# Performance work log

Measured on AMD Instinct MI355X. Metric: run time of the kernel, lower is better.

## Reference

```python
import jax, jax.numpy as jnp
import numpy as np
from jax import lax


def _conv(x, w, b, pad, dil):
    # standard NCHW conv, OIHW weights
    y = lax.conv_general_dilated(x, w, (1, 1), [(pad, pad), (pad, pad)],
                                 rhs_dilation=(dil, dil),
                                 dimension_numbers=('NCHW', 'OIHW', 'NCHW'))
    return y + b[None, :, None, None]


def _bilinear(img, py, px):
    # img: [B,C,H,W]; py,px: [B,KK,H,W] float sample positions.
    # Zero-padding bilinear sampling (torchvision deform_conv semantics):
    # each of the 4 corners contributes 0 if it lies outside the image.
    B, C, H, W = img.shape
    y0 = jnp.floor(py)
    x0 = jnp.floor(px)
    wy1 = py - y0
    wx1 = px - x0
    imgf = img.reshape(B, C, H * W)

    def corner(yi, xi, wgt):
        valid = (yi >= 0) & (yi <= H - 1) & (xi >= 0) & (xi <= W - 1)
        yc = jnp.clip(yi, 0, H - 1).astype(jnp.int32)
        xc = jnp.clip(xi, 0, W - 1).astype(jnp.int32)
        idx = yc * W + xc  # [B,KK,H,W]
        g = jax.vmap(lambda im, ix: jnp.take(im, ix.reshape(-1), axis=1))(imgf, idx)
        g = g.reshape(B, C, *yi.shape[1:])  # [B,C,KK,H,W]
        return g * (wgt * valid.astype(img.dtype))[:, None]

    return (corner(y0, x0, (1 - wy1) * (1 - wx1))
            + corner(y0, x0 + 1, (1 - wy1) * wx1)
            + corner(y0 + 1, x0, wy1 * (1 - wx1))
            + corner(y0 + 1, x0 + 1, wy1 * wx1))


def _deform_dw(x, off_w, off_b, dw_w, K, pad, dil):
    # offset-predicted deformable depthwise conv (groups == channels)
    B, C, H, W = x.shape
    off = _conv(x, off_w, off_b, pad, dil).reshape(B, K * K, 2, H, W)
    dy, dx = off[:, :, 0], off[:, :, 1]  # torchvision order: (dy, dx) per tap
    ky, kx = jnp.meshgrid(jnp.arange(K), jnp.arange(K), indexing='ij')
    by = (ky.reshape(-1) * dil - pad).astype(x.dtype)  # [KK]
    bx = (kx.reshape(-1) * dil - pad).astype(x.dtype)
    py = jnp.arange(H, dtype=x.dtype)[None, None, :, None] + by[None, :, None, None] + dy
    px = jnp.arange(W, dtype=x.dtype)[None, None, None, :] + bx[None, :, None, None] + dx
    s = _bilinear(x, py, px)  # [B,C,KK,H,W]
    return jnp.einsum('bckhw,ck->bchw', s, dw_w.reshape(C, K * K))


def setup_inputs() -> dict:
    key = jax.random.key(0)
    ks = jax.random.split(key, 9)
    B, C, H, W = 4, 64, 56, 56
    f = lambda k, shape, s: jax.random.normal(k, shape, jnp.float32) * s
    return dict(
        x=f(ks[0], (B, C, H, W), 1.0),
        off_w1=f(ks[1], (2 * 5 * 5, C, 5, 5), 0.01), off_b1=f(ks[2], (2 * 5 * 5,), 0.01),
        dw_w1=f(ks[3], (C, 1, 5, 5), 0.1),
        off_w2=f(ks[4], (2 * 7 * 7, C, 7, 7), 0.01), off_b2=f(ks[5], (2 * 7 * 7,), 0.01),
        dw_w2=f(ks[6], (C, 1, 7, 7), 0.1),
        pw_w=f(ks[7], (C, C, 1, 1), 0.05), pw_b=f(ks[8], (C,), 0.05),
    )


def reference(x, off_w1, off_b1, dw_w1, off_w2, off_b2, dw_w2, pw_w, pw_b):
    attn = _deform_dw(x, off_w1, off_b1, dw_w1, 5, 2, 1)       # 5x5 deformable dw
    attn = _deform_dw(attn, off_w2, off_b2, dw_w2, 7, 9, 3)    # 7x7 dil-3 deformable dw
    attn = _conv(attn, pw_w, pw_b, 0, 1)                       # 1x1 pointwise
    return x * attn                                            # gated multiply
```

## Files before the change

### kernel.cpp

```cpp
#include <hip/hip_runtime.h>

#define BB 4
#define CC 64
#define HH 56
#define WW 56
#define HW (HH*WW)

typedef unsigned short u16;
typedef unsigned int u32;
typedef __attribute__((ext_vector_type(8))) short bf16x8;
typedef __attribute__((ext_vector_type(4))) float f32x4;

__device__ __forceinline__ u16 f2bf(float f) {
    union { float f; unsigned u; } c; c.f = f;
    unsigned u = c.u;
    u = (u + 0x7FFFu + ((u >> 16) & 1u)) >> 16;
    return (u16)u;
}
__device__ __forceinline__ float bf2f(u16 v) {
    union { unsigned u; float f; } c; c.u = ((unsigned)v) << 16;
    return c.f;
}
__device__ __forceinline__ float lo_f(u32 u) {
    union { unsigned u; float f; } c; c.u = u << 16; return c.f;
}
__device__ __forceinline__ float hi_f(u32 u) {
    union { unsigned u; float f; } c; c.u = u & 0xffff0000u; return c.f;
}

#define R1 102400
#define R2 401408
#define R3 4096
#define R4 1600
#define R5 3136
#define TGRID (BB*(HW/64))
#define PREPN (R1+R2+R3+R4+R5)
__global__ __launch_bounds__(256)
void prep_tr_kernel(const float* __restrict__ x,
                    const float* __restrict__ ow1, const float* __restrict__ ow2,
                    const float* __restrict__ pw,  const float* __restrict__ dw1,
                    const float* __restrict__ dw2,
                    u16* __restrict__ xT,
                    u16* __restrict__ w2t1, u16* __restrict__ w2t2,
                    u16* __restrict__ pwT, float* __restrict__ dwT1,
                    float* __restrict__ dwT2) {
    __shared__ u16 tile[64][72];
    const int t = threadIdx.x;
    if (blockIdx.x < TGRID) {
        const int blk = blockIdx.x;
        const int b   = blk / (HW/64);
        const int p0  = (blk % (HW/64))*64;
        const int px  = t & 63, icq = t >> 6;
        const float* ip = x + ((size_t)b*CC + icq*16)*HW + p0 + px;
        #pragma unroll
        for (int i = 0; i < 16; ++i)
            tile[px][icq*16 + i] = f2bf(ip[(size_t)i*HW]);
        __syncthreads();
        const int px2 = t >> 2, g = t & 3;
        u16* op = xT + ((size_t)b*HW + p0 + px2)*64 + g*16;
        const uint4* s = (const uint4*)&tile[px2][g*16];
        ((uint4*)op)[0] = s[0];
        ((uint4*)op)[1] = s[1];
        return;
    }
    const int i = (blockIdx.x - TGRID)*256 + t;
    if (i < R1) {
        const int ic = i & 63, n = (i >> 6) & 63, tap = i >> 12;
        w2t1[i] = f2bf((n < 50) ? ow1[((size_t)n*64 + ic)*25 + tap] : 0.f);
    } else if (i < R1+R2) {
        const int j = i - R1;
        const int ic = j & 63, n = (j >> 6) & 127, tap = j >> 13;
        w2t2[j] = f2bf((n < 98) ? ow2[((size_t)n*64 + ic)*49 + tap] : 0.f);
    } else if (i < R1+R2+R3) {
        const int j = i - (R1+R2);
        pwT[j] = f2bf(pw[j]);
    } else if (i < R1+R2+R3+R4) {
        const int j = i - (R1+R2+R3);
        const int c = j & 63, k = j >> 6;
        dwT1[j] = dw1[c*25 + k];
    } else if (i < R1+R2+R3+R4+R5) {
        const int j = i - (R1+R2+R3+R4);
        const int c = j & 63, k = j >> 6;
        dwT2[j] = dw2[c*49 + k];
    }
}

__device__ __forceinline__ uint4 selz(bool v, uint4 a) {
    const uint4 z = make_uint4(0,0,0,0);
    return v ? a : z;
}

template<int K, int DIL, int PAD, int COUT, int NP, int NPAD, int NTW>
__global__ __launch_bounds__(256, 4)
void conv_mfma_lds_kernel(const u16* __restrict__ xT, const u16* __restrict__ w2t,
                          const float* __restrict__ bias, float* __restrict__ out) {
    constexpr int KK = K*K;
    constexpr int BROWS = 16*NTW;
    __shared__ u16 Ab[2][64*64];
    __shared__ u16 Bb[2][BROWS*64];

    const int nm   = HW/64;
    const int b    = blockIdx.x / nm;
    const int p0   = (blockIdx.x % nm)*64;
    const int nt0  = blockIdx.y;
    const int t    = threadIdx.x;
    const int wave = t >> 6;
    const int lane = t & 63;

    const int spx = t >> 3;
    const int sc  = t & 7;
    const int pA  = p0 + spx;
    const int pB  = p0 + spx + 32;
    const int pyA = pA / WW, pxA = pA % WW;
    const int pyB = pB / WW, pxB = pB % WW;
    const u16* xb = xT + (size_t)b*HW*64;
    const int sslotA = ((sc + spx) & 7)*8;
    const int bn  = t >> 3;
    const int bslot = ((sc + bn) & 7)*8;
    const u16* wbase = w2t + (size_t)nt0*BROWS*64;

    const int r = lane & 15, quad = lane >> 4;
    const int mloc = wave*16 + r;
    const int arow = mloc*64;
    const int a0s = ((quad     + mloc) & 7)*8;
    const int a1s = ((quad + 4 + mloc) & 7)*8;
    const int b0s = ((quad     + r) & 7)*8;
    const int b1s = ((quad + 4 + r) & 7)*8;

    f32x4 acc[NTW];
    #pragma unroll
    for (int h = 0; h < NTW; ++h) acc[h] = (f32x4){0.f,0.f,0.f,0.f};
    const uint4 z4 = make_uint4(0,0,0,0);

    auto LD = [&](int tap, uint4& a0, uint4& a1, bool& va, bool& vb, uint4& bb) {
        const int dyy = (tap/K)*DIL - PAD;
        const int dxx = (tap%K)*DIL - PAD;
        const int off = dyy*WW + dxx;
        {
            const int yy = pyA + dyy, xx = pxA + dxx;
            va = ((unsigned)yy < (unsigned)HH) && ((unsigned)xx < (unsigned)WW);
            a0 = *(const uint4*)(xb + (size_t)(va ? (pA + off) : 0)*64 + sc*8);
        }
        {
            const int yy = pyB + dyy, xx = pxB + dxx;
            vb = ((unsigned)yy < (unsigned)HH) && ((unsigned)xx < (unsigned)WW);
            a1 = *(const uint4*)(xb + (size_t)(vb ? (pB + off) : 0)*64 + sc*8);
        }
        if (BROWS == 32 || bn < BROWS)
            bb = *(const uint4*)(wbase + ((size_t)tap*NP + bn)*64 + sc*8);
    };

    uint4 rA0 = z4, rA1 = z4, rB = z4;
    bool v0 = false, v1 = false;
    LD(0, rA0, rA1, v0, v1, rB);

    #pragma unroll
    for (int tap = 0; tap < KK; ++tap) {
        uint4 nA0 = z4, nA1 = z4, nB = z4;
        bool nv0 = false, nv1 = false;
        if (tap + 1 < KK) LD(tap + 1, nA0, nA1, nv0, nv1, nB);

        u16* A  = &Ab[tap & 1][0];
        u16* Bq = &Bb[tap & 1][0];
        *(uint4*)(A + spx*64      + sslotA) = selz(v0, rA0);
        *(uint4*)(A + (spx+32)*64 + sslotA) = selz(v1, rA1);
        if (BROWS == 32 || bn < BROWS) *(uint4*)(Bq + bn*64 + bslot) = rB;
        __syncthreads();

        const bf16x8 av0 = *(const bf16x8*)(A + arow + a0s);
        const bf16x8 av1 = *(const bf16x8*)(A + arow + a1s);
        #pragma unroll
        for (int h = 0; h < NTW; ++h) {
            const int brow = (h*16 + r)*64;
            const bf16x8 bv0 = *(const bf16x8*)(Bq + brow + b0s);
            const bf16x8 bv1 = *(const bf16x8*)(Bq + brow + b1s);
            acc[h] = __builtin_amdgcn_mfma_f32_16x16x32_bf16(av0, bv0, acc[h], 0, 0, 0);
            acc[h] = __builtin_amdgcn_mfma_f32_16x16x32_bf16(av1, bv1, acc[h], 0, 0, 0);
        }

        rA0 = nA0; rA1 = nA1; rB = nB; v0 = nv0; v1 = nv1;
    }

    #pragma unroll
    for (int h = 0; h < NTW; ++h) {
        const int n = nt0*BROWS + h*16 + r;
        if (n < COUT) {
            const float bv = bias[n];
            float* op = out + ((size_t)b*HW + p0 + wave*16 + quad*4)*NPAD + n;
            #pragma unroll
            for (int r2 = 0; r2 < 4; ++r2) op[(size_t)r2*NPAD] = acc[h][r2] + bv;
        }
    }
}

template<int K, int DIL, int PAD, int NPAD>
__global__ __launch_bounds__(256)
void deform_cl_kernel(const u16* __restrict__ inT, const float* __restrict__ offT,
                      const float* __restrict__ dwT, u16* __restrict__ outT) {
    constexpr int KK = K*K;
    __shared__ float4 swt[8][KK];
    __shared__ int4   sat[8][KK];
    __shared__ float  sdw[KK*64];

    const int t = threadIdx.x;
    const int nb8 = (BB*HW/8) >> 3;
    const int blk0 = blockIdx.x;
    const int blk = (blk0 & 7)*nb8 + (blk0 >> 3);
    const int p0 = blk*8;
    const int b  = p0 / HW;
    const int pl0 = p0 - b*HW;

    for (int i = t; i < KK*64; i += 256) sdw[i] = dwT[i];

    for (int i = t; i < 8*KK; i += 256) {
        const int pix = i / KK, k = i - pix*KK;
        const int pl  = pl0 + pix;
        const int h = pl / WW, w = pl % WW;
        const float* orow = offT + ((size_t)b*HW + pl)*NPAD;
        const float dy = orow[2*k];
        const float dx = orow[2*k+1];
        const float py = (float)(h + (k/K)*DIL - PAD) + dy;
        const float px = (float)(w + (k%K)*DIL - PAD) + dx;
        const float y0f = floorf(py), x0f = floorf(px);
        const float wy1 = py - y0f,  wx1 = px - x0f;
        const float wy0 = 1.f - wy1, wx0 = 1.f - wx1;
        const int y0 = (int)y0f, x0 = (int)x0f;

        const int y0c = min(max(y0,   0), HH-1);
        const int y1c = min(max(y0+1, 0), HH-1);
        const int x0c = min(max(x0,   0), WW-1);
        const int x1c = min(max(x0+1, 0), WW-1);
        const float gy0 = wy0 * ((y0   >= 0 && y0   < HH) ? 1.f : 0.f);
        const float gy1 = wy1 * ((y0+1 >= 0 && y0+1 < HH) ? 1.f : 0.f);
        const float gx0 = wx0 * ((x0   >= 0 && x0   < WW) ? 1.f : 0.f);
        const float gx1 = wx1 * ((x0+1 >= 0 && x0+1 < WW) ? 1.f : 0.f);

        swt[pix][k] = make_float4(gy0*gx0, gy0*gx1, gy1*gx0, gy1*gx1);
        const int r0 = y0c*WW, r1 = y1c*WW;
        sat[pix][k] = make_int4((r0 + x0c) << 7, (r0 + x1c) << 7,
                                (r1 + x0c) << 7, (r1 + x1c) << 7);
    }
    __syncthreads();

    const int wave = t >> 6, lane = t & 63;
    const int pixl = 2*wave + (lane >> 5);
    const int chp  = lane & 31;
    const char* ib = (const char*)(inT + (size_t)b*HW*64) + chp*4;

    float accx = 0.f, accy = 0.f;

    int4   av[3];
    float4 wv[2];
    float2 dv[2];
    u32 c00[2], c01[2], c10[2], c11[2];

    av[0] = sat[pixl][0];
    if (KK > 1) av[1] = sat[pixl][1];
    wv[0] = swt[pixl][0];
    dv[0] = *(const float2*)&sdw[2*chp];
    c00[0] = *(const u32*)(ib + av[0].x);
    c01[0] = *(const u32*)(ib + av[0].y);
    c10[0] = *(const u32*)(ib + av[0].z);
    c11[0] = *(const u32*)(ib + av[0].w);

    #pragma unroll
    for (int k = 0; k < KK; ++k) {
        const int kn = k + 1;
        if (kn + 1 < KK) av[(kn+1)%3] = sat[pixl][kn+1];
        if (kn < KK) {
            wv[kn&1] = swt[pixl][kn];
            dv[kn&1] = *(const float2*)&sdw[kn*64 + 2*chp];
            const int4 a = av[kn%3];
            c00[kn&1] = *(const u32*)(ib + a.x);
            c01[kn&1] = *(const u32*)(ib + a.y);
            c10[kn&1] = *(const u32*)(ib + a.z);
            c11[kn&1] = *(const u32*)(ib + a.w);
        }
        const float4 w = wv[k&1];
        const u32 u00 = c00[k&1], u01 = c01[k&1], u10 = c10[k&1], u11 = c11[k&1];
        const float sx = lo_f(u00)*w.x + lo_f(u01)*w.y + lo_f(u10)*w.z + lo_f(u11)*w.w;
        const float sy = hi_f(u00)*w.x + hi_f(u01)*w.y + hi_f(u10)*w.z + hi_f(u11)*w.w;
        const float2 d = dv[k&1];
        accx += sx * d.x;
        accy += sy * d.y;
    }

    const u32 o = (u32)f2bf(accx) | ((u32)f2bf(accy) << 16);
    *(u32*)((char*)outT + (size_t)(p0 + pixl)*128 + chp*4) = o;
}

__global__ __launch_bounds__(256)
void pw_mfma_kernel(const u16* __restrict__ a2T, const u16* __restrict__ pwT,
                    const float* __restrict__ pb, const float* __restrict__ x,
                    float* __restrict__ out) {
    const int nm = HW/64;
    const int b  = blockIdx.x / nm;
    const int p0 = (blockIdx.x % nm)*64 + (threadIdx.x >> 6)*16;
    const int nt = blockIdx.y;
    const int lane = threadIdx.x & 63;
    const int r = lane & 15, quad = lane >> 4;

    const u16* ap = a2T + ((size_t)b*HW + p0 + r)*64 + quad*8;
    f32x4 acc = (f32x4){0.f,0.f,0.f,0.f};
    #pragma unroll
    for (int ks = 0; ks < 2; ++ks) {
        const bf16x8 av = *(const bf16x8*)(ap + ks*32);
        const bf16x8 bv = *(const bf16x8*)(pwT + ((size_t)(nt*16 + r))*64 + ks*32 + quad*8);
        acc = __builtin_amdgcn_mfma_f32_16x16x32_bf16(av, bv, acc, 0, 0, 0);
    }

    const int n = nt*16 + r;
    const float bv = pb[n];
    const size_t base = ((size_t)b*CC + n)*HW + p0 + quad*4;
    #pragma unroll
    for (int r2 = 0; r2 < 4; ++r2)
        out[base + r2] = x[base + r2] * (acc[r2] + bv);
}

template<int K, int DIL, int PAD, int COUT, int OCB>
__global__ __launch_bounds__(256)
void off_conv_sg_kernel(const float* __restrict__ in, const float* __restrict__ wgt,
                        const float* __restrict__ bias, float* __restrict__ out) {
    constexpr int KK = K*K;
    const int nOB = COUT / OCB;
    const int b   = blockIdx.x / nOB;
    const int oc0 = (blockIdx.x % nOB) * OCB;
    const int x   = threadIdx.x;
    const int h   = blockIdx.y*4 + threadIdx.y;

    float acc[OCB];
    #pragma unroll
    for (int o = 0; o < OCB; ++o) acc[o] = bias[oc0+o];

    const float* inb = in + (size_t)b*CC*HW;
    const float* wb  = wgt + (size_t)oc0*CC*KK;

    for (int ic = 0; ic < CC; ++ic) {
        const float* inp = inb + ic*HW;
        const float* wp  = wb + ic*KK;
        #pragma unroll
        for (int ky = 0; ky < K; ++ky) {
            const int  y  = h + ky*DIL - PAD;
            const bool yv = (y >= 0) && (y < HH);
            const int  yc = yv ? y : 0;
            const float* row = inp + yc*WW;
            #pragma unroll
            for (int kx = 0; kx < K; ++kx) {
                const int  xx = x + kx*DIL - PAD;
                const bool v  = yv && (xx >= 0) && (xx < WW);
                const int  xc = (xx < 0) ? 0 : ((xx >= WW) ? (WW-1) : xx);
                float val = row[xc];
                val = v ? val : 0.f;
                const int t = ky*K + kx;
                #pragma unroll
                for (int o = 0; o < OCB; ++o)
                    acc[o] += wp[(size_t)o*CC*KK + t] * val;
            }
        }
    }

    if (x >= WW) return;
    #pragma unroll
    for (int o = 0; o < OCB; ++o)
        out[((size_t)b*COUT + oc0 + o)*HW + h*WW + x] = acc[o];
}

template<int K, int DIL, int PAD>
__global__ __launch_bounds__(64)
void deform_dw_full_kernel(const float* __restrict__ in, const float* __restrict__ off,
                           const float* __restrict__ dw, float* __restrict__ out) {
    constexpr int KK = K*K;
    const int idx = blockIdx.x*64 + threadIdx.x;
    const int x = idx % WW;
    const int h = (idx / WW) % HH;
    const int c = (idx / HW) % CC;
    const int b = idx / (CC*HW);

    const float* inp  = in  + ((size_t)b*CC + c)*HW;
    const float* offp = off + (size_t)b*(2*KK)*HW + h*WW + x;
    const float* dwp  = dw  + c*KK;

    float acc = 0.f;
    #pragma unroll 7
    for (int k = 0; k < KK; ++k) {
        const float dy = offp[(2*k  )*HW];
        const float dx = offp[(2*k+1)*HW];
        const float py = (float)(h + (k/K)*DIL - PAD) + dy;
        const float px = (float)(x + (k%K)*DIL - PAD) + dx;
        const float y0f = floorf(py), x0f = floorf(px);
        const float wy1 = py - y0f,  wx1 = px - x0f;
        const float wy0 = 1.f - wy1, wx0 = 1.f - wx1;
        const int y0 = (int)y0f, x0 = (int)x0f;

        const int y0c = min(max(y0,   0), HH-1);
        const int y1c = min(max(y0+1, 0), HH-1);
        const int x0c = min(max(x0,   0), WW-1);
        const int x1c = min(max(x0+1, 0), WW-1);
        const float my0 = (y0   >= 0 && y0   < HH) ? 1.f : 0.f;
        const float my1 = (y0+1 >= 0 && y0+1 < HH) ? 1.f : 0.f;
        const float mx0 = (x0   >= 0 && x0   < WW) ? 1.f : 0.f;
        const float mx1 = (x0+1 >= 0 && x0+1 < WW) ? 1.f : 0.f;

        const float v00 = inp[y0c*WW + x0c];
        const float v01 = inp[y0c*WW + x1c];
        const float v10 = inp[y1c*WW + x0c];
        const float v11 = inp[y1c*WW + x1c];

        const float gx0 = wx0*mx0, gx1 = wx1*mx1;
        const float s = (v00*gx0 + v01*gx1) * (wy0*my0)
                      + (v10*gx0 + v11*gx1) * (wy1*my1);
        acc += s * dwp[k];
    }
    out[idx] = acc;
}

__global__ __launch_bounds__(256)
void pw_mul_kernel(const float* __restrict__ x, const float* __restrict__ a2,
                   const float* __restrict__ pw, const float* __restrict__ pb,
                   float* __restrict__ out) {
    constexpr int HW4 = HW/4;
    const int t = blockIdx.x*256 + threadIdx.x;
    if (t >= BB*CC*HW4) return;
    const int sp4 = t % HW4;
    const int oc  = (t / HW4) % CC;
    const int b   = t / (CC*HW4);

    const float4* ap = (const float4*)(a2 + (size_t)b*CC*HW) + sp4;
    const float4* wp4 = (const float4*)(pw + oc*CC);
    const float pbv = pb[oc];
    float4 acc = make_float4(pbv, pbv, pbv, pbv);
    #pragma unroll 4
    for (int ic4 = 0; ic4 < CC/4; ++ic4) {
        const float4 w = wp4[ic4];
        float4 a0 = ap[(ic4*4+0)*HW4];
        float4 a1 = ap[(ic4*4+1)*HW4];
        float4 a2v = ap[(ic4*4+2)*HW4];
        float4 a3 = ap[(ic4*4+3)*HW4];
        acc.x += w.x*a0.x + w.y*a1.x + w.z*a2v.x + w.w*a3.x;
        acc.y += w.x*a0.y + w.y*a1.y + w.z*a2v.y + w.w*a3.y;
        acc.z += w.x*a0.z + w.y*a1.z + w.z*a2v.z + w.w*a3.z;
        acc.w += w.x*a0.w + w.y*a1.w + w.z*a2v.w + w.w*a3.w;
    }
    const float4 xv = ((const float4*)x)[t];
    float4 r;
    r.x = xv.x*acc.x; r.y = xv.y*acc.y; r.z = xv.z*acc.z; r.w = xv.w*acc.w;
    ((float4*)out)[t] = r;
}

extern "C" void kernel_launch(void* const* d_in, const int* in_sizes, int n_in,
                              void* d_out, int out_size, void* d_ws, size_t ws_size,
                              hipStream_t stream) {
    const float* x      = (const float*)d_in[0];
    const float* off_w1 = (const float*)d_in[1];
    const float* off_b1 = (const float*)d_in[2];
    const float* dw_w1  = (const float*)d_in[3];
    const float* off_w2 = (const float*)d_in[4];
    const float* off_b2 = (const float*)d_in[5];
    const float* dw_w2  = (const float*)d_in[6];
    const float* pw_w   = (const float*)d_in[7];
    const float* pw_b   = (const float*)d_in[8];
    float* out = (float*)d_out;

    const size_t nF    = (size_t)BB*CC*HW;
    const size_t attnB = nF*sizeof(float);
    const size_t off2B = (size_t)BB*98*HW*sizeof(float);
    const size_t offTB = (size_t)BB*HW*112*sizeof(float);
    const size_t chB   = (size_t)BB*HW*64*sizeof(u16);
    char* ws = (char*)d_ws;

    const int n    = (int)nF;
    const int dbl  = n/64;
    const int pbl  = (n/4 + 255)/256;
    dim3 cblk(64,4);
    dim3 rgrd1(BB*(50/5), HH/4);
    dim3 rgrd2(BB*(98/7), HH/4);
    dim3 cgrd1(TGRID, 2);
    dim3 cgrd2(TGRID, 4);
    dim3 pgrd(TGRID, 4);
    const int dgrid = BB*HW/8;

    const size_t oOFF  = 0;
    const size_t oXT   = oOFF + offTB;
    const size_t oA1T  = oXT  + chB;
    const size_t oA2T  = oA1T + chB;
    const size_t oW1   = oA2T + chB;
    const size_t oW2   = oW1  + (size_t)R1*2;
    const size_t oPWT  = oW2  + (size_t)R2*2;
    const size_t oDW1  = oPWT + (size_t)R3*2;
    const size_t oDW2  = oDW1 + (size_t)R4*4;
    const size_t TOT   = oDW2 + (size_t)R5*4;

    if (ws_size >= TOT) {
        float* off_buf = (float*)(ws + oOFF);
        u16*   xT      = (u16*)(ws + oXT);
        u16*   a1T     = (u16*)(ws + oA1T);
        u16*   a2T     = (u16*)(ws + oA2T);
        u16*   w2t1    = (u16*)(ws + oW1);
        u16*   w2t2    = (u16*)(ws + oW2);
        u16*   pwT     = (u16*)(ws + oPWT);
        float* dwT1    = (float*)(ws + oDW1);
        float* dwT2    = (float*)(ws + oDW2);

        prep_tr_kernel<<<TGRID + (PREPN+255)/256, 256, 0, stream>>>(
            x, off_w1, off_w2, pw_w, dw_w1, dw_w2,
            xT, w2t1, w2t2, pwT, dwT1, dwT2);

        conv_mfma_lds_kernel<5,1,2,50,64,64,2><<<cgrd1, 256, 0, stream>>>(xT, w2t1, off_b1, off_buf);
        deform_cl_kernel<5,1,2,64><<<dgrid, 256, 0, stream>>>(xT, off_buf, dwT1, a1T);

        conv_mfma_lds_kernel<7,3,9,98,128,112,2><<<cgrd2, 256, 0, stream>>>(a1T, w2t2, off_b2, off_buf);
        deform_cl_kernel<7,3,9,112><<<dgrid, 256, 0, stream>>>(a1T, off_buf, dwT2, a2T);

        pw_mfma_kernel<<<pgrd, 256, 0, stream>>>(a2T, pwT, pw_b, x, out);
    } else if (ws_size >= off2B + attnB) {
        float* off_buf = (float*)ws;
        float* attn1   = (float*)d_out;
        float* attn2   = (float*)(ws + off2B);
        off_conv_sg_kernel<5,1,2,50,5><<<rgrd1, cblk, 0, stream>>>(x, off_w1, off_b1, off_buf);
        deform_dw_full_kernel<5,1,2><<<dbl, 64, 0, stream>>>(x, off_buf, dw_w1, attn1);
        off_conv_sg_kernel<7,3,9,98,7><<<rgrd2, cblk, 0, stream>>>(attn1, off_w2, off_b2, off_buf);
        deform_dw_full_kernel<7,3,9><<<dbl, 64, 0, stream>>>(attn1, off_buf, dw_w2, attn2);
        pw_mul_kernel<<<pbl, 256, 0, stream>>>(x, attn2, pw_w, pw_b, out);
    } else {
        float* attn1 = (float*)d_out;
        float* attn2 = (float*)ws;
        float* off1  = (float*)ws;
        off_conv_sg_kernel<5,1,2,50,5><<<rgrd1, cblk, 0, stream>>>(x, off_w1, off_b1, off1);
        deform_dw_full_kernel<5,1,2><<<dbl, 64, 0, stream>>>(x, off1, dw_w1, attn1);
        float* off2 = (float*)(ws + attnB);
        off_conv_sg_kernel<7,3,9,98,7><<<rgrd2, cblk, 0, stream>>>(attn1, off_w2, off_b2, off2);
        deform_dw_full_kernel<7,3,9><<<dbl, 64, 0, stream>>>(attn1, off2, dw_w2, attn2);
        pw_mul_kernel<<<pbl, 256, 0, stream>>>(x, attn2, pw_w, pw_b, out);
    }
}
```

Baseline: 157.0 us.

## Zero-pad channel-last activations and stage conv tiles via direct global-to-LDS loads

Activations are stored in spatially zero-padded channel-last buffers, with the border zeroing folded into the prep kernel, so the offset conv no longer needs per-tap bounds checks or select-to-zero. The conv loader uses global_load_lds to copy A and B tiles straight into LDS, with the XOR swizzle applied on the global address side. This drops the register staging and the explicit LDS stores. The deform kernels are templated to read and write the padded layouts. The trade-offs are a larger workspace, extra zeroing work, and a sync placement that is now one barrier per tap after the MFMA.

```diff
diff --git a/kernel.cpp b/kernel.cpp
--- a/kernel.cpp
+++ b/kernel.cpp
@@ -17,30 +17,39 @@
     u = (u + 0x7FFFu + ((u >> 16) & 1u)) >> 16;
     return (u16)u;
 }
-__device__ __forceinline__ float bf2f(u16 v) {
-    union { unsigned u; float f; } c; c.u = ((unsigned)v) << 16;
-    return c.f;
-}
 __device__ __forceinline__ float lo_f(u32 u) {
     union { unsigned u; float f; } c; c.u = u << 16; return c.f;
 }
 __device__ __forceinline__ float hi_f(u32 u) {
     union { unsigned u; float f; } c; c.u = u & 0xffff0000u; return c.f;
 }
+
+typedef const __attribute__((address_space(1))) unsigned int guint;
+typedef __attribute__((address_space(3))) unsigned int luint;
+__device__ __forceinline__ void gl_lds16(const void* g, void* l) {
+    __builtin_amdgcn_global_load_lds((guint*)g, (luint*)l, 16, 0, 0);
+}
+
+#define W1P 60
+#define PB1 3600
+#define W2P 74
+#define PB2 5476
 
 #define R1 102400
 #define R2 401408
 #define R3 4096
 #define R4 1600
 #define R5 3136
+#define R6z (BB*PB1*8)
+#define R7z (BB*PB2*8)
 #define TGRID (BB*(HW/64))
-#define PREPN (R1+R2+R3+R4+R5)
+#define PREPN (R1+R2+R3+R4+R5+R6z+R7z)
 __global__ __launch_bounds__(256)
 void prep_tr_kernel(const float* __restrict__ x,
                     const float* __restrict__ ow1, const float* __restrict__ ow2,
                     const float* __restrict__ pw,  const float* __restrict__ dw1,
                     const float* __restrict__ dw2,
-                    u16* __restrict__ xT,
+                    u16* __restrict__ xTp, u16* __restrict__ a1Tp,
                     u16* __restrict__ w2t1, u16* __restrict__ w2t2,
                     u16* __restrict__ pwT, float* __restrict__ dwT1,
                     float* __restrict__ dwT2) {
@@ -57,7 +66,9 @@
             tile[px][icq*16 + i] = f2bf(ip[(size_t)i*HW]);
         __syncthreads();
         const int px2 = t >> 2, g = t & 3;
-        u16* op = xT + ((size_t)b*HW + p0 + px2)*64 + g*16;
+        const int p = p0 + px2;
+        const int y = p / WW, xw = p % WW;
+        u16* op = xTp + ((size_t)b*PB1 + (y+2)*W1P + (xw+2))*64 + g*16;
         const uint4* s = (const uint4*)&tile[px2][g*16];
         ((uint4*)op)[0] = s[0];
         ((uint4*)op)[1] = s[1];
@@ -82,20 +93,31 @@
         const int j = i - (R1+R2+R3+R4);
         const int c = j & 63, k = j >> 6;
         dwT2[j] = dw2[c*49 + k];
-    }
-}
-
-__device__ __forceinline__ uint4 selz(bool v, uint4 a) {
-    const uint4 z = make_uint4(0,0,0,0);
-    return v ? a : z;
+    } else if (i < R1+R2+R3+R4+R5+R6z) {
+        const int j = i - (R1+R2+R3+R4+R5);
+        const int c8 = j & 7, q = j >> 3;
+        const int px = q % PB1, bz = q / PB1;
+        const int y = px / W1P, xx = px % W1P;
+        if (y < 2 || y >= 58 || xx < 2 || xx >= 58)
+            *(uint4*)(xTp + ((size_t)bz*PB1 + px)*64 + c8*8) = make_uint4(0,0,0,0);
+    } else if (i < PREPN) {
+        const int j = i - (R1+R2+R3+R4+R5+R6z);
+        const int c8 = j & 7, q = j >> 3;
+        const int px = q % PB2, bz = q / PB2;
+        const int y = px / W2P, xx = px % W2P;
+        if (y < 9 || y >= 65 || xx < 9 || xx >= 65)
+            *(uint4*)(a1Tp + ((size_t)bz*PB2 + px)*64 + c8*8) = make_uint4(0,0,0,0);
+    }
 }
 
 template<int K, int DIL, int PAD, int COUT, int NP, int NPAD, int NTW>
 __global__ __launch_bounds__(256, 4)
-void conv_mfma_lds_kernel(const u16* __restrict__ xT, const u16* __restrict__ w2t,
+void conv_mfma_lds_kernel(const u16* __restrict__ xTp, const u16* __restrict__ w2t,
                           const float* __restrict__ bias, float* __restrict__ out) {
     constexpr int KK = K*K;
     constexpr int BROWS = 16*NTW;
+    constexpr int WP  = WW + 2*PAD;
+    constexpr int IPB = (HH + 2*PAD)*WP;
     __shared__ u16 Ab[2][64*64];
     __shared__ u16 Bb[2][BROWS*64];
 
@@ -109,15 +131,15 @@
 
     const int spx = t >> 3;
     const int sc  = t & 7;
+    const int gk8 = ((sc - spx) & 7)*8;
     const int pA  = p0 + spx;
-    const int pB  = p0 + spx + 32;
+    const int pB  = pA + 32;
     const int pyA = pA / WW, pxA = pA % WW;
     const int pyB = pB / WW, pxB = pB % WW;
-    const u16* xb = xT + (size_t)b*HW*64;
-    const int sslotA = ((sc + spx) & 7)*8;
-    const int bn  = t >> 3;
-    const int bslot = ((sc + bn) & 7)*8;
-    const u16* wbase = w2t + (size_t)nt0*BROWS*64;
+    const u16* xb  = xTp + (size_t)b*IPB*64;
+    const u16* gA0 = xb + ((size_t)((pyA+PAD)*WP + (pxA+PAD)))*64 + gk8;
+    const u16* gA1 = xb + ((size_t)((pyB+PAD)*WP + (pxB+PAD)))*64 + gk8;
+    const u16* gB  = w2t + (size_t)nt0*BROWS*64 + spx*64 + gk8;
 
     const int r = lane & 15, quad = lane >> 4;
     const int mloc = wave*16 + r;
@@ -130,43 +152,25 @@
     f32x4 acc[NTW];
     #pragma unroll
     for (int h = 0; h < NTW; ++h) acc[h] = (f32x4){0.f,0.f,0.f,0.f};
-    const uint4 z4 = make_uint4(0,0,0,0);
-
-    auto LD = [&](int tap, uint4& a0, uint4& a1, bool& va, bool& vb, uint4& bb) {
+
+    auto ISSUE = [&](int tap, int buf) {
         const int dyy = (tap/K)*DIL - PAD;
         const int dxx = (tap%K)*DIL - PAD;
-        const int off = dyy*WW + dxx;
-        {
-            const int yy = pyA + dyy, xx = pxA + dxx;
-            va = ((unsigned)yy < (unsigned)HH) && ((unsigned)xx < (unsigned)WW);
-            a0 = *(const uint4*)(xb + (size_t)(va ? (pA + off) : 0)*64 + sc*8);
-        }
-        {
-            const int yy = pyB + dyy, xx = pxB + dxx;
-            vb = ((unsigned)yy < (unsigned)HH) && ((unsigned)xx < (unsigned)WW);
-            a1 = *(const uint4*)(xb + (size_t)(vb ? (pB + off) : 0)*64 + sc*8);
-        }
-        if (BROWS == 32 || bn < BROWS)
-            bb = *(const uint4*)(wbase + ((size_t)tap*NP + bn)*64 + sc*8);
+        const int toff = (dyy*WP + dxx)*64;
+        gl_lds16(gA0 + toff,           &Ab[buf][wave*512]);
+        gl_lds16(gA1 + toff,           &Ab[buf][2048 + wave*512]);
+        gl_lds16(gB + tap*(NP*64),     &Bb[buf][wave*512]);
     };
 
-    uint4 rA0 = z4, rA1 = z4, rB = z4;
-    bool v0 = false, v1 = false;
-    LD(0, rA0, rA1, v0, v1, rB);
+    ISSUE(0, 0);
+    __syncthreads();
 
     #pragma unroll
     for (int tap = 0; tap < KK; ++tap) {
-        uint4 nA0 = z4, nA1 = z4, nB = z4;
-        bool nv0 = false, nv1 = false;
-        if (tap + 1 < KK) LD(tap + 1, nA0, nA1, nv0, nv1, nB);
-
-        u16* A  = &Ab[tap & 1][0];
-        u16* Bq = &Bb[tap & 1][0];
-        *(uint4*)(A + spx*64      + sslotA) = selz(v0, rA0);
-        *(uint4*)(A + (spx+32)*64 + sslotA) = selz(v1, rA1);
-        if (BROWS == 32 || bn < BROWS) *(uint4*)(Bq + bn*64 + bslot) = rB;
-        __syncthreads();
-
+        if (tap + 1 < KK) ISSUE(tap + 1, (tap + 1) & 1);
+
+        const u16* A  = &Ab[tap & 1][0];
+        const u16* Bq = &Bb[tap & 1][0];
         const bf16x8 av0 = *(const bf16x8*)(A + arow + a0s);
         const bf16x8 av1 = *(const bf16x8*)(A + arow + a1s);
         #pragma unroll
@@ -177,8 +181,7 @@
             acc[h] = __builtin_amdgcn_mfma_f32_16x16x32_bf16(av0, bv0, acc[h], 0, 0, 0);
             acc[h] = __builtin_amdgcn_mfma_f32_16x16x32_bf16(av1, bv1, acc[h], 0, 0, 0);
         }
-
-        rA0 = nA0; rA1 = nA1; rB = nB; v0 = nv0; v1 = nv1;
+        __syncthreads();
     }
 
     #pragma unroll
@@ -193,7 +196,8 @@
     }
 }
 
-template<int K, int DIL, int PAD, int NPAD>
+template<int K, int DIL, int PAD, int NPAD,
+         int IP, int IWP, int IPB, int OP, int OWP, int OPB>
 __global__ __launch_bounds__(256)
 void deform_cl_kernel(const u16* __restrict__ inT, const float* __restrict__ offT,
                       const float* __restrict__ dwT, u16* __restrict__ outT) {
@@ -236,16 +240,16 @@
         const float gx1 = wx1 * ((x0+1 >= 0 && x0+1 < WW) ? 1.f : 0.f);
 
         swt[pix][k] = make_float4(gy0*gx0, gy0*gx1, gy1*gx0, gy1*gx1);
-        const int r0 = y0c*WW, r1 = y1c*WW;
-        sat[pix][k] = make_int4((r0 + x0c) << 7, (r0 + x1c) << 7,
-                                (r1 + x0c) << 7, (r1 + x1c) << 7);
+        const int r0 = (y0c + IP)*IWP, r1 = (y1c + IP)*IWP;
+        sat[pix][k] = make_int4((r0 + x0c + IP) << 7, (r0 + x1c + IP) << 7,
+                                (r1 + x0c + IP) << 7, (r1 + x1c + IP) << 7);
     }
     __syncthreads();
 
     const int wave = t >> 6, lane = t & 63;
     const int pixl = 2*wave + (lane >> 5);
     const int chp  = lane & 31;
-    const char* ib = (const char*)(inT + (size_t)b*HW*64) + chp*4;
+    const char* ib = (const char*)(inT + (size_t)b*IPB*64) + chp*4;
 
     float accx = 0.f, accy = 0.f;
 
@@ -285,8 +289,10 @@
         accy += sy * d.y;
     }
 
+    const int oy = (pl0 + pixl) / WW, ox = (pl0 + pixl) % WW;
+    const int opx = (oy + OP)*OWP + (ox + OP);
     const u32 o = (u32)f2bf(accx) | ((u32)f2bf(accy) << 16);
-    *(u32*)((char*)outT + (size_t)(p0 + pixl)*128 + chp*4) = o;
+    *(u32*)((char*)outT + ((size_t)b*OPB + opx)*128 + chp*4) = o;
 }
 
 __global__ __launch_bounds__(256)
@@ -466,6 +472,8 @@
     const size_t off2B = (size_t)BB*98*HW*sizeof(float);
     const size_t offTB = (size_t)BB*HW*112*sizeof(float);
     const size_t chB   = (size_t)BB*HW*64*sizeof(u16);
+    const size_t xpB   = (size_t)BB*PB1*64*sizeof(u16);
+    const size_t a1pB  = (size_t)BB*PB2*64*sizeof(u16);
     char* ws = (char*)d_ws;
 
     const int n    = (int)nF;
@@ -480,20 +488,20 @@
     const int dgrid = BB*HW/8;
 
     const size_t oOFF  = 0;
-    const size_t oXT   = oOFF + offTB;
-    const size_t oA1T  = oXT  + chB;
-    const size_t oA2T  = oA1T + chB;
-    const size_t oW1   = oA2T + chB;
-    const size_t oW2   = oW1  + (size_t)R1*2;
-    const size_t oPWT  = oW2  + (size_t)R2*2;
-    const size_t oDW1  = oPWT + (size_t)R3*2;
-    const size_t oDW2  = oDW1 + (size_t)R4*4;
-    const size_t TOT   = oDW2 + (size_t)R5*4;
+    const size_t oXTP  = oOFF  + offTB;
+    const size_t oA1TP = oXTP  + xpB;
+    const size_t oA2T  = oA1TP + a1pB;
+    const size_t oW1   = oA2T  + chB;
+    const size_t oW2   = oW1   + (size_t)R1*2;
+    const size_t oPWT  = oW2   + (size_t)R2*2;
+    const size_t oDW1  = oPWT  + (size_t)R3*2;
+    const size_t oDW2  = oDW1  + (size_t)R4*4;
+    const size_t TOT   = oDW2  + (size_t)R5*4;
 
     if (ws_size >= TOT) {
         float* off_buf = (float*)(ws + oOFF);
-        u16*   xT      = (u16*)(ws + oXT);
-        u16*   a1T     = (u16*)(ws + oA1T);
+        u16*   xTp     = (u16*)(ws + oXTP);
+        u16*   a1Tp    = (u16*)(ws + oA1TP);
         u16*   a2T     = (u16*)(ws + oA2T);
         u16*   w2t1    = (u16*)(ws + oW1);
         u16*   w2t2    = (u16*)(ws + oW2);
@@ -503,13 +511,13 @@
 
         prep_tr_kernel<<<TGRID + (PREPN+255)/256, 256, 0, stream>>>(
             x, off_w1, off_w2, pw_w, dw_w1, dw_w2,
-            xT, w2t1, w2t2, pwT, dwT1, dwT2);
-
-        conv_mfma_lds_kernel<5,1,2,50,64,64,2><<<cgrd1, 256, 0, stream>>>(xT, w2t1, off_b1, off_buf);
-        deform_cl_kernel<5,1,2,64><<<dgrid, 256, 0, stream>>>(xT, off_buf, dwT1, a1T);
-
-        conv_mfma_lds_kernel<7,3,9,98,128,112,2><<<cgrd2, 256, 0, stream>>>(a1T, w2t2, off_b2, off_buf);
-        deform_cl_kernel<7,3,9,112><<<dgrid, 256, 0, stream>>>(a1T, off_buf, dwT2, a2T);
+            xTp, a1Tp, w2t1, w2t2, pwT, dwT1, dwT2);
+
+        conv_mfma_lds_kernel<5,1,2,50,64,64,2><<<cgrd1, 256, 0, stream>>>(xTp, w2t1, off_b1, off_buf);
+        deform_cl_kernel<5,1,2,64, 2,W1P,PB1, 9,W2P,PB2><<<dgrid, 256, 0, stream>>>(xTp, off_buf, dwT1, a1Tp);
+
+        conv_mfma_lds_kernel<7,3,9,98,128,112,2><<<cgrd2, 256, 0, stream>>>(a1Tp, w2t2, off_b2, off_buf);
+        deform_cl_kernel<7,3,9,112, 9,W2P,PB2, 0,WW,HW><<<dgrid, 256, 0, stream>>>(a1Tp, off_buf, dwT2, a2T);
 
         pw_mfma_kernel<<<pgrd, 256, 0, stream>>>(a2T, pwT, pw_b, x, out);
     } else if (ws_size >= off2B + attnB) {
```

New measurement: 162.1 us. +3.3%, slower.
